# Optimization experiments

Hardware: AMD Instinct MI355X
Metric: run time of the kernel (lower is better)

## Reference

```python
import jax, jax.numpy as jnp
from jax import lax
import numpy as np

DN = ('NCHW', 'OIHW', 'NCHW')


def _conv(x, w, b, padding='SAME'):
    y = lax.conv_general_dilated(x, w, (1, 1), padding, dimension_numbers=DN)
    return y + b[None, :, None, None]


def _lrn(x, size=2, alpha=2e-5, beta=0.75, k=1.0):
    # torch LocalResponseNorm(size=2): pad channels left by size//2=1, avg-pool
    # window of 2 over channels (count_include_pad), so div[c]=(x[c-1]^2+x[c]^2)/2
    sq = x * x
    p = jnp.pad(sq, ((0, 0), (1, 0), (0, 0), (0, 0)))
    avg = (p[:, :-1] + p[:, 1:]) * 0.5
    return x / (k + alpha * avg) ** beta


def _maxpool2(x):
    return lax.reduce_window(x, -jnp.inf, lax.max, (1, 1, 2, 2), (1, 1, 2, 2), 'VALID')


def _interweave(i1, i2, i3, i4):
    # rows1: even rows <- i1, odd rows <- i2 ; rows2: i3/i4
    # columns: even cols <- rows1, odd cols <- rows2
    B, C, H, W = i1.shape
    r1 = jnp.stack([i1, i2], axis=3).reshape(B, C, 2 * H, W)
    r2 = jnp.stack([i3, i4], axis=3).reshape(B, C, 2 * H, W)
    return jnp.stack([r1, r2], axis=4).reshape(B, C, 2 * H, 2 * W)


def setup_inputs() -> dict:
    key = jax.random.key(0)
    ks = jax.random.split(key, 16)

    def w(k, shape):
        fan_in = shape[1] * shape[2] * shape[3]
        return jax.random.normal(k, shape, jnp.float32) * np.float32((2.0 / fan_in) ** 0.5)

    return {
        'x': jax.random.normal(ks[0], (2, 1, 128, 128), jnp.float32),
        'w1': w(ks[1], (64, 1, 7, 7)),    'b1': jnp.zeros((64,), jnp.float32),
        'w2': w(ks[2], (64, 64, 5, 5)),   'b2': jnp.zeros((64,), jnp.float32),
        'w3': w(ks[3], (64, 64, 3, 3)),   'b3': jnp.zeros((64,), jnp.float32),
        'w4': w(ks[4], (64, 64, 3, 3)),   'b4': jnp.zeros((64,), jnp.float32),
        'w5': w(ks[5], (1024, 64, 16, 16)), 'b5': jnp.zeros((1024,), jnp.float32),
        'w6': w(ks[6], (1024, 1024, 1, 1)), 'b6': jnp.zeros((1024,), jnp.float32),
        'w7': w(ks[7], (1, 1024, 1, 1)),    'b7': jnp.zeros((1,), jnp.float32),
    }


def reference(x, w1, b1, w2, b2, w3, b3, w4, b4, w5, b5, w6, b6, w7, b7):
    h = jax.nn.relu(_conv(x, w1, b1))
    h = jax.nn.relu(_conv(h, w2, b2))
    h = _lrn(h)
    B = x.shape[0]
    # 4 shifted crops, stacked along batch -> one pass through the shared stack
    crops = jnp.concatenate([
        h[:, :, :-1, :-1], h[:, :, 1:, :-1],
        h[:, :, :-1, 1:],  h[:, :, 1:, 1:],
    ], axis=0)
    y = _maxpool2(crops)
    y = jax.nn.relu(_conv(y, w3, b3))
    y = jax.nn.relu(_conv(y, w4, b4))
    y = _lrn(y)
    y = jax.nn.relu(_conv(y, w5, b5, 'VALID'))
    y = jax.nn.relu(_conv(y, w6, b6, 'VALID'))
    y = jax.nn.sigmoid(_conv(y, w7, b7, 'VALID'))
    i1, i2, i3, i4 = y[:B], y[B:2 * B], y[2 * B:3 * B], y[3 * B:]
    return _interweave(i1, i2, i3, i4)
```

## Files before the change

kernel.cpp:

```cpp
#include <hip/hip_runtime.h>

typedef unsigned short u16;
typedef unsigned int   u32;
typedef unsigned long long u64;
typedef short short8 __attribute__((ext_vector_type(8)));
typedef float f32x4  __attribute__((ext_vector_type(4)));

__device__ __forceinline__ u16 f2bf(float f){
  u32 u = __float_as_uint(f);
  u32 r = (u + 0x7fffu + ((u >> 16) & 1u)) >> 16;
  return (u16)r;
}
__device__ __forceinline__ float lrn_one(float v, float pv){
  float avg = 0.5f*(v*v + pv*pv);
  float d = 1.0f + 2e-5f*avg;
  return v * exp2f(-0.75f * log2f(d));
}

__global__ __launch_bounds__(256) void k0w5(const float* __restrict__ w5, u16* __restrict__ wpk){
  int idx = blockIdx.x*256 + threadIdx.x;
  int j     =  idx        & 7;
  int oc128 = (idx >> 3)  & 127;
  int quad  = (idx >> 10) & 3;
  int kx    = (idx >> 12) & 15;
  int chunk = (idx >> 16) & 31;
  int ocb   =  idx >> 21;
  int oc = ocb*128 + oc128;
  int ic = chunk*2 + (quad>>1);
  int ky = (quad&1)*8 + j;
  wpk[idx] = f2bf(w5[((oc*64 + ic)*16 + ky)*16 + kx]);
}

__global__ __launch_bounds__(256) void k0w6(const float* __restrict__ w6, u16* __restrict__ wpk){
  int idx = blockIdx.x*256 + threadIdx.x;
  int j     =  idx        & 7;
  int oc128 = (idx >> 3)  & 127;
  int quad  = (idx >> 10) & 3;
  int kk    = (idx >> 12) & 3;
  int kc    = (idx >> 14) & 7;
  int mb    =  idx >> 17;
  int oc = mb*128 + oc128;
  int ic = kc*128 + kk*32 + quad*8 + j;
  wpk[idx] = f2bf(w6[oc*1024 + ic]);
}

__global__ __launch_bounds__(256) void k0z(float* __restrict__ accum){
  int idx = blockIdx.x*256 + threadIdx.x;
  if (idx < 18432) accum[idx] = 0.f;
}

__global__ __launch_bounds__(256) void k1_conv7x7(const float* __restrict__ x, const float* __restrict__ w1,
                                                  const float* __restrict__ b1, float* __restrict__ out){
  int idx = blockIdx.x*256 + threadIdx.x;
  int ox = idx & 127, oy = (idx>>7)&127, oc = (idx>>14)&63, n = idx>>20;
  float acc = b1[oc];
  const float* wb = w1 + oc*49;
  const float* xb = x + n*16384;
  #pragma unroll
  for (int ky=0;ky<7;++ky){
    int y = oy + ky - 3;
    if ((unsigned)y < 128u){
      #pragma unroll
      for (int kx=0;kx<7;++kx){
        int xx = ox + kx - 3;
        if ((unsigned)xx < 128u)
          acc += wb[ky*7+kx] * xb[y*128+xx];
      }
    }
  }
  out[idx] = acc > 0.f ? acc : 0.f;
}

__global__ __launch_bounds__(256) void k2_conv5x5(const float* __restrict__ in, const float* __restrict__ w2,
                                                  const float* __restrict__ b2, float* __restrict__ out){
  __shared__ __align__(16) float t[1360];
  __shared__ float wl[200];
  int bid = blockIdx.x;
  int colg = bid & 1;
  int rowg = (bid >> 1) & 7;
  int ocg  = (bid >> 4) & 7;
  int n    =  bid >> 7;
  int tid = threadIdx.x;
  int oy0 = rowg*16, ox0 = colg*64;
  int r = tid >> 4, c0 = (tid & 15)*4;
  float acc[8][4];
  #pragma unroll
  for (int o=0;o<8;++o)
    #pragma unroll
    for (int p=0;p<4;++p) acc[o][p] = 0.f;

  for (int ic=0; ic<64; ++ic){
    __syncthreads();
    for (int u=tid; u<1360; u+=256){
      int rr = u/68, cc = u - rr*68;
      int gy = oy0+rr-2, gx = ox0+cc-2;
      t[u] = ((unsigned)gy<128u && (unsigned)gx<128u) ? in[((n*64+ic)*128+gy)*128+gx] : 0.f;
    }
    if (tid < 200) wl[tid] = w2[((ocg*8 + tid/25)*64 + ic)*25 + (tid%25)];
    __syncthreads();
    #pragma unroll
    for (int ky=0;ky<5;++ky){
      float4 a = *(const float4*)&t[(r+ky)*68 + c0];
      float4 b = *(const float4*)&t[(r+ky)*68 + c0 + 4];
      float f[8] = {a.x,a.y,a.z,a.w,b.x,b.y,b.z,b.w};
      #pragma unroll
      for (int o=0;o<8;++o){
        #pragma unroll
        for (int kx=0;kx<5;++kx){
          float wv = wl[o*25 + ky*5 + kx];
          #pragma unroll
          for (int p=0;p<4;++p) acc[o][p] += wv * f[kx+p];
        }
      }
    }
  }
  #pragma unroll
  for (int o=0;o<8;++o){
    float bb = b2[ocg*8 + o];
    float4 st;
    st.x = fmaxf(acc[o][0]+bb, 0.f);
    st.y = fmaxf(acc[o][1]+bb, 0.f);
    st.z = fmaxf(acc[o][2]+bb, 0.f);
    st.w = fmaxf(acc[o][3]+bb, 0.f);
    *(float4*)&out[((n*64 + ocg*8 + o)*128 + oy0+r)*128 + ox0 + c0] = st;
  }
}

__global__ __launch_bounds__(256) void k3_lrn_crop_pool(const float* __restrict__ h, float* __restrict__ out){
  int idx = blockIdx.x*256 + threadIdx.x;
  int j = idx % 63; int t1 = idx / 63;
  int i = t1 % 63; int t2 = t1 / 63;
  int c = t2 & 63; int b = t2 >> 6;
  int v = b >> 1, n = b & 1;
  int r0 = v & 1, c0 = v >> 1;
  const float* base  = h + ((n*64+c  )*128)*128;
  const float* basep = h + ((n*64+c-1)*128)*128;
  float m = -3.4e38f;
  #pragma unroll
  for (int a=0;a<2;++a)
    #pragma unroll
    for (int bb=0;bb<2;++bb){
      int y = r0+2*i+a, xx = c0+2*j+bb;
      float val = base[y*128+xx];
      float pv  = c ? basep[y*128+xx] : 0.f;
      m = fmaxf(m, lrn_one(val, pv));
    }
  out[idx] = m;
}

__global__ __launch_bounds__(256) void k_conv3x3(const float* __restrict__ in, const float* __restrict__ w,
                                                 const float* __restrict__ bias, float* __restrict__ out){
  __shared__ __align__(16) float t[408];
  __shared__ float wl[72];
  int bid = blockIdx.x;
  int rowg = bid & 15;
  int ocg  = (bid >> 4) & 7;
  int b    =  bid >> 7;
  int tid = threadIdx.x;
  int r = tid >> 6, cx = tid & 63;
  int oy0 = rowg*4;
  float acc[8];
  #pragma unroll
  for (int o=0;o<8;++o) acc[o] = 0.f;

  for (int ic=0; ic<64; ++ic){
    __syncthreads();
    #pragma unroll
    for (int u0=0; u0<2; ++u0){
      int u = tid + u0*256;
      if (u < 408){
        int rr = u/68, cc = u - rr*68;
        int gy = oy0+rr-1, gx = cc-1;
        t[u] = (cc<66 && (unsigned)gy<63u && (unsigned)gx<63u) ? in[((b*64+ic)*63+gy)*63+gx] : 0.f;
      }
    }
    if (tid < 72) wl[tid] = w[((ocg*8 + tid/9)*64 + ic)*9 + (tid%9)];
    __syncthreads();
    #pragma unroll
    for (int ky=0;ky<3;++ky){
      float a0 = t[(r+ky)*68 + cx];
      float a1 = t[(r+ky)*68 + cx + 1];
      float a2 = t[(r+ky)*68 + cx + 2];
      #pragma unroll
      for (int o=0;o<8;++o){
        acc[o] += wl[o*9+ky*3  ]*a0;
        acc[o] += wl[o*9+ky*3+1]*a1;
        acc[o] += wl[o*9+ky*3+2]*a2;
      }
    }
  }
  int oy = oy0 + r;
  if (oy < 63 && cx < 63){
    #pragma unroll
    for (int o=0;o<8;++o){
      float v = acc[o] + bias[ocg*8+o];
      out[((b*64 + ocg*8 + o)*63 + oy)*63 + cx] = v > 0.f ? v : 0.f;
    }
  }
}

__global__ __launch_bounds__(256) void k6_lrn_bf(const float* __restrict__ in, u16* __restrict__ outb){
  int idx = blockIdx.x*256+threadIdx.x;
  int col = idx & 63, iy = (idx>>6)&63, ic = (idx>>12)&63, b = idx>>18;
  u16 o = 0;
  if (col < 63 && iy < 63){
    int src = ((b*64+ic)*63 + iy)*63 + col;
    float v  = in[src];
    float pv = ic ? in[src - 3969] : 0.f;
    o = f2bf(lrn_one(v, pv));
  }
  outb[idx] = o;
}

__global__ __launch_bounds__(192, 1) void k7u(const u16* __restrict__ inb, const u16* __restrict__ wpk,
                                              const float* __restrict__ b5, u16* __restrict__ y5){
  __shared__ __align__(16) u16 itile[7168];
  int bid = blockIdx.x;
  int och = bid & 15;
  int rem = bid >> 4;
  int n8  = rem & 7;
  int r   = rem >> 3;
  int tid = threadIdx.x;
  int w = tid / 64, lane = tid & 63, quad = lane >> 4, m = lane & 15;
  int ic2q = quad >> 1, kyh = quad & 1;

  f32x4 acc[4][6];
  #pragma unroll
  for (int tm=0;tm<4;++tm)
    #pragma unroll
    for (int t=0;t<6;++t) acc[tm][t] = (f32x4){0.f,0.f,0.f,0.f};

  const u16* gin    = inb + ((size_t)n8 * 64) * 4096;
  const u16* wblock = wpk + ((size_t)(och >> 1) << 21) + (och & 1)*512;
  const u16* wbase  = wblock + quad*1024 + m*8;

  int bb = ((ic2q*7 + (2*w + kyh))*64 + m)*8;

  short8 af[4][4];
  short8 bf[2][6];
  #pragma unroll
  for (int q=0;q<4;++q) af[0][q] = *(const short8*)(wbase + q*128);
  #pragma unroll
  for (int q=0;q<4;++q) af[1][q] = *(const short8*)(wbase + 4096 + q*128);

  #pragma unroll 1
  for (int chunk=0; chunk<32; ++chunk){
    __syncthreads();
    {
      const u16* gq = gin + (size_t)(chunk*2)*4096 + r*64;
      for (int v = tid; v < 1792; v += 192){
        int cp  = v & 31;
        int t2  = v >> 5;
        int iyp = t2 % 28;
        int ic2 = t2 / 28;
        int iy0 = iyp*2;
        const u16* g = gq + ic2*4096 + iy0*64 + 2*cp;
        u32 d0 = *(const u32*)(g);
        u32 d1 = *(const u32*)(g + 64);
        u32 lo = (d0 & 0xffffu) | (d1 << 16);
        u32 hi = (d0 >> 16) | (d1 & 0xffff0000u);
        int win = iy0 >> 3, j = iy0 & 7;
        int base = ((ic2*7 + win)*64 + 2*cp)*8 + j;
        *(u32*)&itile[base]     = lo;
        *(u32*)&itile[base + 8] = hi;
      }
    }
    __syncthreads();
    const u16* wk0  = wbase + (chunk << 16);
    const u16* bptr = itile + bb;

    #pragma unroll
    for (int t=0;t<6;++t) bf[0][t] = *(const short8*)(bptr + (t%3)*128 + (t/3)*512);

    #pragma unroll
    for (int kx=0; kx<16; ++kx){
      #pragma unroll
      for (int q=0;q<4;++q) af[(kx+2)&3][q] = *(const short8*)(wk0 + (kx+2)*4096 + q*128);
      if (kx < 15){
        #pragma unroll
        for (int t=0;t<6;++t) bf[(kx+1)&1][t] = *(const short8*)(bptr + (t%3)*128 + (t/3)*512 + (kx+1)*8);
      }
      __builtin_amdgcn_s_setprio(1);
      #pragma unroll
      for (int q=0;q<4;++q)
        #pragma unroll
        for (int t=0;t<6;++t)
          acc[q][t] = __builtin_amdgcn_mfma_f32_16x16x32_bf16(af[kx&3][q], bf[kx&1][t], acc[q][t], 0, 0, 0);
      __builtin_amdgcn_s_setprio(0);
    }
  }

  #pragma unroll
  for (int tm=0;tm<4;++tm){
    #pragma unroll
    for (int rr=0;rr<4;++rr){
      int oc = och*64 + tm*16 + quad*4 + rr;
      float bias = b5[oc];
      #pragma unroll
      for (int t=0;t<6;++t){
        int row = r + 16*w + 8*(t/3);
        int ox  = (t%3)*16 + m;
        float v = acc[tm][t][rr] + bias;
        v = v>0.f ? v : 0.f;
        y5[(((size_t)n8*1024 + oc)*48 + row)*48 + ox] = f2bf(v);
      }
    }
  }
}

__global__ __launch_bounds__(128) void k8a(const u16* __restrict__ y5, const u16* __restrict__ w6pk,
                                           const float* __restrict__ b6, const float* __restrict__ w7,
                                           float* __restrict__ accum){
  __shared__ __align__(16) u16 btile[96*136];
  __shared__ float red[8*96];
  int bid = blockIdx.x;
  int mb = bid & 7;
  int r  = bid >> 3;
  int n8 = r / 24, rp = r % 24;
  int r0 = 2*rp;
  int tid = threadIdx.x;
  int w = tid >> 6, lane = tid & 63, quad = lane >> 4, m = lane & 15;

  f32x4 acc[4][6];
  #pragma unroll
  for (int tm=0;tm<4;++tm)
    #pragma unroll
    for (int t=0;t<6;++t) acc[tm][t] = (f32x4){0.f,0.f,0.f,0.f};

  #pragma unroll 1
  for (int kc=0; kc<8; ++kc){
    __syncthreads();
    for (int u=tid; u<6144; u+=128){
      int pp = u % 48; int ic2 = u / 48;
      int rowl = pp / 24; int ox0 = (pp % 24)*2;
      u32 val = *(const u32*)(y5 + (((size_t)(n8*1024 + kc*128 + ic2)*48) + r0 + rowl)*48 + ox0);
      int px = rowl*48 + ox0;
      btile[(px  )*136 + ic2] = (u16)(val & 0xffffu);
      btile[(px+1)*136 + ic2] = (u16)(val >> 16);
    }
    __syncthreads();
    #pragma unroll 1
    for (int kk=0; kk<4; ++kk){
      short8 af[4];
      #pragma unroll
      for (int tm=0;tm<4;++tm)
        af[tm] = *(const short8*)(w6pk + (size_t)((((mb*8 + kc)*4 + kk)*4 + quad)*128 + (w*64 + tm*16 + m))*8);
      short8 bf[6];
      #pragma unroll
      for (int t=0;t<6;++t){
        int pxl = ((t>=3)?48:0) + (t%3)*16 + m;
        bf[t] = *(const short8*)(btile + pxl*136 + kk*32 + quad*8);
      }
      #pragma unroll
      for (int tm=0;tm<4;++tm)
        #pragma unroll
        for (int t=0;t<6;++t)
          acc[tm][t] = __builtin_amdgcn_mfma_f32_16x16x32_bf16(af[tm], bf[t], acc[tm][t], 0, 0, 0);
    }
  }
  float part[6];
  #pragma unroll
  for (int t=0;t<6;++t) part[t]=0.f;
  #pragma unroll
  for (int tm=0;tm<4;++tm){
    #pragma unroll
    for (int rr=0;rr<4;++rr){
      int oc = mb*128 + w*64 + tm*16 + quad*4 + rr;
      float bb = b6[oc];
      float ww = w7[oc];
      #pragma unroll
      for (int t=0;t<6;++t){
        float z = acc[tm][t][rr] + bb;
        z = z>0.f ? z : 0.f;
        part[t] += ww*z;
      }
    }
  }
  #pragma unroll
  for (int t=0;t<6;++t){
    int pxl = ((t>=3)?48:0) + (t%3)*16 + m;
    red[(w*4+quad)*96 + pxl] = part[t];
  }
  __syncthreads();
  if (tid < 96){
    float s = 0.f;
    #pragma unroll
    for (int k=0;k<8;++k) s += red[k*96 + tid];
    int rowl = tid / 48, ox = tid % 48;
    atomicAdd(&accum[((size_t)n8*48 + r0 + rowl)*48 + ox], s);
  }
}

__global__ __launch_bounds__(256) void k8b(const float* __restrict__ accum, const float* __restrict__ b7,
                                           float* __restrict__ out){
  int idx = blockIdx.x*256 + threadIdx.x;
  if (idx >= 18432) return;
  int n8 = idx / 2304; int rem = idx % 2304;
  int oy = rem / 48, ox = rem % 48;
  float s = accum[idx] + b7[0];
  float sig = 1.f / (1.f + expf(-s));
  int v = n8 >> 1, n = n8 & 1;
  int a = v & 1, bcol = v >> 1;
  out[((size_t)n*96 + 2*oy + a)*96 + 2*ox + bcol] = sig;
}

extern "C" void kernel_launch(void* const* d_in, const int* in_sizes, int n_in,
                              void* d_out, int out_size, void* d_ws, size_t ws_size,
                              hipStream_t stream){
  const float* x  = (const float*)d_in[0];
  const float* w1 = (const float*)d_in[1];
  const float* b1 = (const float*)d_in[2];
  const float* w2 = (const float*)d_in[3];
  const float* b2 = (const float*)d_in[4];
  const float* w3 = (const float*)d_in[5];
  const float* b3 = (const float*)d_in[6];
  const float* w4 = (const float*)d_in[7];
  const float* b4 = (const float*)d_in[8];
  const float* w5 = (const float*)d_in[9];
  const float* b5 = (const float*)d_in[10];
  const float* w6 = (const float*)d_in[11];
  const float* b6 = (const float*)d_in[12];
  const float* w7 = (const float*)d_in[13];
  const float* b7 = (const float*)d_in[14];
  float* ws = (float*)d_ws;
  float* out = (float*)d_out;

  float* C  = ws;
  u16*   Cb = (u16*)ws;
  float* A  = ws + 2097152;
  float* B  = ws + 4194304;
  u16*   F    = (u16*)(ws + 2097152);
  u16*   Wpk5 = (u16*)(ws + 11534336);
  u16*   W6pk = (u16*)(ws + 19922944);
  float* accum = ws + 20447232;

  hipLaunchKernelGGL(k0w5,            dim3(65536), dim3(256), 0, stream, w5, Wpk5);
  hipLaunchKernelGGL(k0w6,            dim3(4096),  dim3(256), 0, stream, w6, W6pk);
  hipLaunchKernelGGL(k0z,             dim3(72),    dim3(256), 0, stream, accum);
  hipLaunchKernelGGL(k1_conv7x7,      dim3(8192),  dim3(256), 0, stream, x, w1, b1, A);
  hipLaunchKernelGGL(k2_conv5x5,      dim3(256),   dim3(256), 0, stream, A, w2, b2, B);
  hipLaunchKernelGGL(k3_lrn_crop_pool,dim3(7938),  dim3(256), 0, stream, B, C);
  hipLaunchKernelGGL(k_conv3x3,       dim3(1024),  dim3(256), 0, stream, C, w3, b3, A);
  hipLaunchKernelGGL(k_conv3x3,       dim3(1024),  dim3(256), 0, stream, A, w4, b4, B);
  hipLaunchKernelGGL(k6_lrn_bf,       dim3(8192),  dim3(256), 0, stream, B, Cb);
  hipLaunchKernelGGL(k7u,             dim3(1024),  dim3(192), 0, stream, Cb, Wpk5, b5, F);
  hipLaunchKernelGGL(k8a,             dim3(1536),  dim3(128), 0, stream, F, W6pk, b6, w7, accum);
  hipLaunchKernelGGL(k8b,             dim3(72),    dim3(256), 0, stream, accum, b7, out);
}
```

Measured before the change: 1.432 ms.

## Double-buffer k7 input tile, retile conv5x5 to more blocks, simplify k8a staging

```diff
diff --git a/kernel.cpp b/kernel.cpp
--- a/kernel.cpp
+++ b/kernel.cpp
@@ -73,26 +73,24 @@
 
 __global__ __launch_bounds__(256) void k2_conv5x5(const float* __restrict__ in, const float* __restrict__ w2,
                                                   const float* __restrict__ b2, float* __restrict__ out){
-  __shared__ __align__(16) float t[1360];
+  __shared__ __align__(16) float t[720];
   __shared__ float wl[200];
   int bid = blockIdx.x;
-  int colg = bid & 1;
-  int rowg = (bid >> 1) & 7;
-  int ocg  = (bid >> 4) & 7;
-  int n    =  bid >> 7;
+  int colg = bid & 3;
+  int rowg = (bid >> 2) & 7;
+  int ocg  = (bid >> 5) & 7;
+  int n    =  bid >> 8;
   int tid = threadIdx.x;
-  int oy0 = rowg*16, ox0 = colg*64;
-  int r = tid >> 4, c0 = (tid & 15)*4;
-  float acc[8][4];
-  #pragma unroll
-  for (int o=0;o<8;++o)
-    #pragma unroll
-    for (int p=0;p<4;++p) acc[o][p] = 0.f;
+  int oy0 = rowg*16, ox0 = colg*32;
+  int r = tid >> 4, c0 = (tid & 15)*2;
+  float acc[8][2];
+  #pragma unroll
+  for (int o=0;o<8;++o){ acc[o][0]=0.f; acc[o][1]=0.f; }
 
   for (int ic=0; ic<64; ++ic){
     __syncthreads();
-    for (int u=tid; u<1360; u+=256){
-      int rr = u/68, cc = u - rr*68;
+    for (int u=tid; u<720; u+=256){
+      int rr = u/36, cc = u - rr*36;
       int gy = oy0+rr-2, gx = ox0+cc-2;
       t[u] = ((unsigned)gy<128u && (unsigned)gx<128u) ? in[((n*64+ic)*128+gy)*128+gx] : 0.f;
     }
@@ -100,16 +98,17 @@
     __syncthreads();
     #pragma unroll
     for (int ky=0;ky<5;++ky){
-      float4 a = *(const float4*)&t[(r+ky)*68 + c0];
-      float4 b = *(const float4*)&t[(r+ky)*68 + c0 + 4];
-      float f[8] = {a.x,a.y,a.z,a.w,b.x,b.y,b.z,b.w};
+      float2 a = *(const float2*)&t[(r+ky)*36 + c0];
+      float2 b = *(const float2*)&t[(r+ky)*36 + c0 + 2];
+      float2 c = *(const float2*)&t[(r+ky)*36 + c0 + 4];
+      float f[6] = {a.x,a.y,b.x,b.y,c.x,c.y};
       #pragma unroll
       for (int o=0;o<8;++o){
         #pragma unroll
         for (int kx=0;kx<5;++kx){
           float wv = wl[o*25 + ky*5 + kx];
-          #pragma unroll
-          for (int p=0;p<4;++p) acc[o][p] += wv * f[kx+p];
+          acc[o][0] += wv * f[kx];
+          acc[o][1] += wv * f[kx+1];
         }
       }
     }
@@ -117,12 +116,10 @@
   #pragma unroll
   for (int o=0;o<8;++o){
     float bb = b2[ocg*8 + o];
-    float4 st;
+    float2 st;
     st.x = fmaxf(acc[o][0]+bb, 0.f);
     st.y = fmaxf(acc[o][1]+bb, 0.f);
-    st.z = fmaxf(acc[o][2]+bb, 0.f);
-    st.w = fmaxf(acc[o][3]+bb, 0.f);
-    *(float4*)&out[((n*64 + ocg*8 + o)*128 + oy0+r)*128 + ox0 + c0] = st;
+    *(float2*)&out[((n*64 + ocg*8 + o)*128 + oy0+r)*128 + ox0 + c0] = st;
   }
 }
 
@@ -212,9 +209,9 @@
   outb[idx] = o;
 }
 
-__global__ __launch_bounds__(192, 1) void k7u(const u16* __restrict__ inb, const u16* __restrict__ wpk,
+__global__ __launch_bounds__(192, 1) void k7v(const u16* __restrict__ inb, const u16* __restrict__ wpk,
                                               const float* __restrict__ b5, u16* __restrict__ y5){
-  __shared__ __align__(16) u16 itile[7168];
+  __shared__ __align__(16) u16 itile[2][7168];
   int bid = blockIdx.x;
   int och = bid & 15;
   int rem = bid >> 4;
@@ -236,6 +233,47 @@
 
   int bb = ((ic2q*7 + (2*w + kyh))*64 + m)*8;
 
+  int goff[10]; int sbase[10];
+  #pragma unroll
+  for (int s=0;s<10;++s){
+    int v = tid + 192*s;
+    if (v < 1792){
+      int cp  = v & 31;
+      int t2  = v >> 5;
+      int iyp = t2 % 28;
+      int ic2 = t2 / 28;
+      int iy0 = iyp*2;
+      goff[s]  = ic2*4096 + iy0*64 + 2*cp + r*64;
+      int win = iy0 >> 3, j = iy0 & 7;
+      sbase[s] = ((ic2*7 + win)*64 + 2*cp)*8 + j;
+    } else { goff[s] = 0; sbase[s] = 0; }
+  }
+
+  u32 sd0[10], sd1[10];
+  auto issue_stage = [&](int chunk2){
+    const u16* gq = gin + (size_t)(chunk2*2)*4096;
+    #pragma unroll
+    for (int s=0;s<10;++s){
+      if (tid + 192*s < 1792){
+        const u16* g = gq + goff[s];
+        sd0[s] = *(const u32*)(g);
+        sd1[s] = *(const u32*)(g + 64);
+      }
+    }
+  };
+  auto write_stage = [&](u16* tl2){
+    #pragma unroll
+    for (int s=0;s<10;++s){
+      if (tid + 192*s < 1792){
+        u32 d0 = sd0[s], d1 = sd1[s];
+        u32 lo = (d0 & 0xffffu) | (d1 << 16);
+        u32 hi = (d0 >> 16) | (d1 & 0xffff0000u);
+        *(u32*)&tl2[sbase[s]]     = lo;
+        *(u32*)&tl2[sbase[s] + 8] = hi;
+      }
+    }
+  };
+
   short8 af[4][4];
   short8 bf[2][6];
   #pragma unroll
@@ -243,31 +281,16 @@
   #pragma unroll
   for (int q=0;q<4;++q) af[1][q] = *(const short8*)(wbase + 4096 + q*128);
 
+  issue_stage(0);
+  write_stage(itile[0]);
+  __syncthreads();
+
   #pragma unroll 1
   for (int chunk=0; chunk<32; ++chunk){
-    __syncthreads();
-    {
-      const u16* gq = gin + (size_t)(chunk*2)*4096 + r*64;
-      for (int v = tid; v < 1792; v += 192){
-        int cp  = v & 31;
-        int t2  = v >> 5;
-        int iyp = t2 % 28;
-        int ic2 = t2 / 28;
-        int iy0 = iyp*2;
-        const u16* g = gq + ic2*4096 + iy0*64 + 2*cp;
-        u32 d0 = *(const u32*)(g);
-        u32 d1 = *(const u32*)(g + 64);
-        u32 lo = (d0 & 0xffffu) | (d1 << 16);
-        u32 hi = (d0 >> 16) | (d1 & 0xffff0000u);
-        int win = iy0 >> 3, j = iy0 & 7;
-        int base = ((ic2*7 + win)*64 + 2*cp)*8 + j;
-        *(u32*)&itile[base]     = lo;
-        *(u32*)&itile[base + 8] = hi;
-      }
-    }
-    __syncthreads();
+    const u16* tl = itile[chunk & 1];
+    if (chunk < 31) issue_stage(chunk+1);
     const u16* wk0  = wbase + (chunk << 16);
-    const u16* bptr = itile + bb;
+    const u16* bptr = tl + bb;
 
     #pragma unroll
     for (int t=0;t<6;++t) bf[0][t] = *(const short8*)(bptr + (t%3)*128 + (t/3)*512);
@@ -287,6 +310,11 @@
         for (int t=0;t<6;++t)
           acc[q][t] = __builtin_amdgcn_mfma_f32_16x16x32_bf16(af[kx&3][q], bf[kx&1][t], acc[q][t], 0, 0, 0);
       __builtin_amdgcn_s_setprio(0);
+    }
+
+    if (chunk < 31){
+      write_stage(itile[(chunk+1) & 1]);
+      __syncthreads();
     }
   }
 
@@ -330,16 +358,22 @@
   #pragma unroll 1
   for (int kc=0; kc<8; ++kc){
     __syncthreads();
-    for (int u=tid; u<6144; u+=128){
-      int pp = u % 48; int ic2 = u / 48;
-      int rowl = pp / 24; int ox0 = (pp % 24)*2;
-      u32 val = *(const u32*)(y5 + (((size_t)(n8*1024 + kc*128 + ic2)*48) + r0 + rowl)*48 + ox0);
-      int px = rowl*48 + ox0;
-      btile[(px  )*136 + ic2] = (u16)(val & 0xffffu);
-      btile[(px+1)*136 + ic2] = (u16)(val >> 16);
-    }
-    __syncthreads();
-    #pragma unroll 1
+    {
+      int pp = tid, ic2 = 0;
+      while (pp >= 48){ pp -= 48; ic2 += 1; }
+      #pragma unroll 1
+      for (int it=0; it<48; ++it){
+        int rowl = (pp >= 24) ? 1 : 0;
+        int ox0  = (pp - rowl*24)*2;
+        u32 val = *(const u32*)(y5 + (((size_t)(n8*1024 + kc*128 + ic2)*48) + r0 + rowl)*48 + ox0);
+        int px = rowl*48 + ox0;
+        btile[(px  )*136 + ic2] = (u16)(val & 0xffffu);
+        btile[(px+1)*136 + ic2] = (u16)(val >> 16);
+        ic2 += 2; pp += 32;
+        if (pp >= 48){ pp -= 48; ic2 += 1; }
+      }
+    }
+    __syncthreads();
     for (int kk=0; kk<4; ++kk){
       short8 af[4];
       #pragma unroll
@@ -438,12 +472,12 @@
   hipLaunchKernelGGL(k0w6,            dim3(4096),  dim3(256), 0, stream, w6, W6pk);
   hipLaunchKernelGGL(k0z,             dim3(72),    dim3(256), 0, stream, accum);
   hipLaunchKernelGGL(k1_conv7x7,      dim3(8192),  dim3(256), 0, stream, x, w1, b1, A);
-  hipLaunchKernelGGL(k2_conv5x5,      dim3(256),   dim3(256), 0, stream, A, w2, b2, B);
+  hipLaunchKernelGGL(k2_conv5x5,      dim3(512),   dim3(256), 0, stream, A, w2, b2, B);
   hipLaunchKernelGGL(k3_lrn_crop_pool,dim3(7938),  dim3(256), 0, stream, B, C);
   hipLaunchKernelGGL(k_conv3x3,       dim3(1024),  dim3(256), 0, stream, C, w3, b3, A);
   hipLaunchKernelGGL(k_conv3x3,       dim3(1024),  dim3(256), 0, stream, A, w4, b4, B);
   hipLaunchKernelGGL(k6_lrn_bf,       dim3(8192),  dim3(256), 0, stream, B, Cb);
-  hipLaunchKernelGGL(k7u,             dim3(1024),  dim3(192), 0, stream, Cb, Wpk5, b5, F);
+  hipLaunchKernelGGL(k7v,             dim3(1024),  dim3(192), 0, stream, Cb, Wpk5, b5, F);
   hipLaunchKernelGGL(k8a,             dim3(1536),  dim3(128), 0, stream, F, W6pk, b6, w7, accum);
   hipLaunchKernelGGL(k8b,             dim3(72),    dim3(256), 0, stream, accum, b7, out);
 }
```

Result: faster. 1.387 ms (-3.2%).
